# Optimization experiments

Measured on AMD Instinct MI355X. Metric: run time of the kernel, lower is better.

## Reference

```python
import jax, jax.numpy as jnp
import numpy as np

N_EMBD = 2048
N_HEAD = 16
N_KV_HEAD = 4
HEAD_DIM = N_EMBD // N_HEAD  # 128
N_REP = N_HEAD // N_KV_HEAD  # 4
ROPE_BASE = 1000000.0
B, T = 2, 2048


def _rotate_half(x):
    x1, x2 = jnp.split(x, 2, axis=-1)
    return jnp.concatenate([-x2, x1], axis=-1)


def _rope(q, k, t):
    # q: [b,t,h,d], k: [b,t,kvh,d]; full rotary (partial_rotary_factor=1.0)
    pos = jnp.arange(t, dtype=jnp.float32)
    inv_freq = 1.0 / (ROPE_BASE ** (jnp.arange(0, HEAD_DIM, 2, dtype=jnp.float32) / HEAD_DIM))
    ang = pos[:, None] * inv_freq[None, :]                      # [t, d/2]
    cos = jnp.concatenate([jnp.cos(ang), jnp.cos(ang)], -1)     # [t, d]
    sin = jnp.concatenate([jnp.sin(ang), jnp.sin(ang)], -1)
    cos = cos[None, :, None, :]
    sin = sin[None, :, None, :]
    q = q * cos + _rotate_half(q) * sin
    k = k * cos + _rotate_half(k) * sin
    return q, k


def setup_inputs() -> dict:
    key = jax.random.key(0)
    ks = jax.random.split(key, 9)
    std = 0.02
    proj_std = 0.02 / np.sqrt(2 * 24)
    return {
        "x": jax.random.normal(ks[0], (B, T, N_EMBD), dtype=jnp.float32),
        "Wq": jax.random.normal(ks[1], (N_EMBD, N_HEAD * HEAD_DIM), dtype=jnp.float32) * std,
        "bq": jnp.zeros((N_HEAD * HEAD_DIM,), dtype=jnp.float32),
        "Wk": jax.random.normal(ks[2], (N_EMBD, N_KV_HEAD * HEAD_DIM), dtype=jnp.float32) * std,
        "bk": jnp.zeros((N_KV_HEAD * HEAD_DIM,), dtype=jnp.float32),
        "Wv": jax.random.normal(ks[3], (N_EMBD, N_KV_HEAD * HEAD_DIM), dtype=jnp.float32) * std,
        "bv": jnp.zeros((N_KV_HEAD * HEAD_DIM,), dtype=jnp.float32),
        "Wo": jax.random.normal(ks[4], (N_EMBD, N_EMBD), dtype=jnp.float32) * proj_std,
        "bo": jnp.zeros((N_EMBD,), dtype=jnp.float32),
    }


def reference(x, Wq, bq, Wk, bk, Wv, bv, Wo, bo):
    b, t, _ = x.shape
    q = (x @ Wq + bq).reshape(b, t, N_HEAD, HEAD_DIM)
    k = (x @ Wk + bk).reshape(b, t, N_KV_HEAD, HEAD_DIM)
    v = (x @ Wv + bv).reshape(b, t, N_KV_HEAD, HEAD_DIM)
    q, k = _rope(q, k, t)
    # repeat_kv: expand kv heads by n_rep
    k = jnp.broadcast_to(k[:, :, :, None, :], (b, t, N_KV_HEAD, N_REP, HEAD_DIM)).reshape(b, t, N_HEAD, HEAD_DIM)
    v = jnp.broadcast_to(v[:, :, :, None, :], (b, t, N_KV_HEAD, N_REP, HEAD_DIM)).reshape(b, t, N_HEAD, HEAD_DIM)
    qh = q.transpose(0, 2, 1, 3)  # [b,h,t,d]
    kh = k.transpose(0, 2, 1, 3)
    vh = v.transpose(0, 2, 1, 3)
    causal = jnp.tril(jnp.ones((t, t), dtype=bool))[None, None]  # [1,1,t,t]
    bias = jnp.where(causal, 0.0, -1e9).astype(jnp.float32)
    scores = jnp.einsum('bhtd,bhTd->bhtT', qh, kh) / jnp.sqrt(jnp.float32(HEAD_DIM))
    attn_w = jax.nn.softmax(scores + bias, axis=-1)
    attn_out = jnp.einsum('bhtT,bhTd->bhtd', attn_w, vh)
    attn = attn_out.transpose(0, 2, 1, 3).reshape(b, t, N_EMBD)
    return attn @ Wo + bo
```

## Files before the change

### kernel.cpp

```cpp
#include <hip/hip_runtime.h>

typedef _Float16 f16x8 __attribute__((ext_vector_type(8)));
typedef _Float16 f16x4 __attribute__((ext_vector_type(4)));
typedef float    f32x4 __attribute__((ext_vector_type(4)));
typedef float    f32x16 __attribute__((ext_vector_type(16)));
typedef unsigned int u32;
typedef unsigned int u32x2 __attribute__((ext_vector_type(2)));
typedef unsigned int u32x4 __attribute__((ext_vector_type(4)));

__device__ __forceinline__ void gload16(const void* g, void* l) {
  __builtin_amdgcn_global_load_lds((const __attribute__((address_space(1))) void*)g,
                                   (__attribute__((address_space(3))) void*)l, 16, 0, 0);
}

__global__ __launch_bounds__(256) void cast_f32_f16(const float* __restrict__ src,
                                                    _Float16* __restrict__ dst, int n4) {
  int i = blockIdx.x * 256 + threadIdx.x;
  if (i < n4) {
    f32x4 v = *(const f32x4*)(src + (size_t)i * 4);
    f16x4 o;
    o[0] = (_Float16)v[0]; o[1] = (_Float16)v[1];
    o[2] = (_Float16)v[2]; o[3] = (_Float16)v[3];
    *(f16x4*)(dst + (size_t)i * 4) = o;
  }
}

__global__ __launch_bounds__(256) void wqkvtrans_kernel(const float* __restrict__ Wq,
                                                        const float* __restrict__ Wk,
                                                        const float* __restrict__ Wv,
                                                        _Float16* __restrict__ dst) {
  const int n0 = blockIdx.x * 64, k0 = blockIdx.y * 64;
  const float* src; int N, nb;
  if (n0 < 2048)      { src = Wq; N = 2048; nb = n0; }
  else if (n0 < 2560) { src = Wk; N = 512;  nb = n0 - 2048; }
  else                { src = Wv; N = 512;  nb = n0 - 2560; }
  __shared__ float tile[64][65];
#pragma unroll
  for (int i = 0; i < 16; ++i) {
    int id = i * 256 + threadIdx.x;
    int kk = id >> 6, nn = id & 63;
    tile[kk][nn] = src[(size_t)(k0 + kk) * N + nb + nn];
  }
  __syncthreads();
#pragma unroll
  for (int i = 0; i < 16; ++i) {
    int id = i * 256 + threadIdx.x;
    int nn = id >> 6, kk = id & 63;
    dst[(size_t)(n0 + nn) * 2048 + k0 + kk] = (_Float16)tile[kk][nn];
  }
}

__global__ __launch_bounds__(256) void wtrans_kernel(const float* __restrict__ src,
                                                     _Float16* __restrict__ dst,
                                                     int N, int K, int rowOff, int ldDst) {
  const int n0 = blockIdx.x * 64, k0 = blockIdx.y * 64;
  __shared__ float tile[64][65];
#pragma unroll
  for (int i = 0; i < 16; ++i) {
    int id = i * 256 + threadIdx.x;
    int kk = id >> 6, nn = id & 63;
    tile[kk][nn] = src[(size_t)(k0 + kk) * N + n0 + nn];
  }
  __syncthreads();
#pragma unroll
  for (int i = 0; i < 16; ++i) {
    int id = i * 256 + threadIdx.x;
    int nn = id >> 6, kk = id & 63;
    dst[(size_t)(rowOff + n0 + nn) * ldDst + k0 + kk] = (_Float16)tile[kk][nn];
  }
}

__global__ __launch_bounds__(256) void biaspack_kernel(const float* __restrict__ bq,
                                                       const float* __restrict__ bk,
                                                       const float* __restrict__ bv,
                                                       float* __restrict__ out) {
  int i = blockIdx.x * 256 + threadIdx.x;
  if (i < 3072) out[i] = (i < 2048) ? bq[i] : (i < 2560 ? bk[i - 2048] : bv[i - 2560]);
}

__global__ void zeroctr_kernel(int* c) { *c = 0; }

template <bool F16OUT>
__global__ __launch_bounds__(256) void gemm_nt(const _Float16* __restrict__ A,
                                               const _Float16* __restrict__ B,
                                               const float* __restrict__ bias,
                                               void* __restrict__ Cv,
                                               int M, int N, int K) {
  __shared__ __align__(16) _Float16 As[128][64];
  __shared__ __align__(16) _Float16 Bs[128][64];
  const int tid = threadIdx.x;
  const int lane = tid & 63, wave = tid >> 6;
  const int wr = wave >> 1, wc = wave & 1;
  const int r = lane & 15, g = lane >> 4;
  const int rb = blockIdx.y * 128, cb = blockIdx.x * 128;

  const int swz = ((tid & 7) ^ ((tid >> 3) & 7)) * 8;
  const _Float16* aSrc = A + (size_t)(rb + (tid >> 3)) * K + swz;
  const _Float16* bSrc = B + (size_t)(cb + (tid >> 3)) * K + swz;

  f32x4 acc[4][4] = {};

  for (int kt = 0; kt < K; kt += 64) {
    __syncthreads();
#pragma unroll
    for (int p = 0; p < 4; ++p) {
      gload16(aSrc + (size_t)(p * 32) * K + kt, (_Float16*)As + (p * 256 + wave * 64) * 8);
      gload16(bSrc + (size_t)(p * 32) * K + kt, (_Float16*)Bs + (p * 256 + wave * 64) * 8);
    }
    __syncthreads();
#pragma unroll
    for (int kk = 0; kk < 2; ++kk) {
      f16x8 af[4], bf[4];
#pragma unroll
      for (int m = 0; m < 4; ++m) {
        int row = wr * 64 + m * 16 + r;
        af[m] = *(const f16x8*)(&As[row][((kk * 4 + g) ^ (row & 7)) * 8]);
      }
#pragma unroll
      for (int n = 0; n < 4; ++n) {
        int row = wc * 64 + n * 16 + r;
        bf[n] = *(const f16x8*)(&Bs[row][((kk * 4 + g) ^ (row & 7)) * 8]);
      }
#pragma unroll
      for (int m = 0; m < 4; ++m)
#pragma unroll
        for (int n = 0; n < 4; ++n)
          acc[m][n] = __builtin_amdgcn_mfma_f32_16x16x32_f16(af[m], bf[n], acc[m][n], 0, 0, 0);
    }
  }

  float bvals[4];
#pragma unroll
  for (int n = 0; n < 4; ++n) bvals[n] = bias[cb + wc * 64 + n * 16 + r];
#pragma unroll
  for (int m = 0; m < 4; ++m) {
#pragma unroll
    for (int n = 0; n < 4; ++n) {
#pragma unroll
      for (int j = 0; j < 4; ++j) {
        int row = rb + wr * 64 + m * 16 + g * 4 + j;
        int col = cb + wc * 64 + n * 16 + r;
        float v = acc[m][n][j] + bvals[n];
        if (F16OUT)
          ((_Float16*)Cv)[(size_t)row * N + col] = (_Float16)v;
        else
          ((float*)Cv)[(size_t)row * N + col] = v;
      }
    }
  }
}

__global__ __launch_bounds__(256) void rope_kernel(_Float16* __restrict__ QKV) {
  const int tok = blockIdx.x;
  const int t = tok & 2047;
  __shared__ float cs[64], sn[64];
  if (threadIdx.x < 64) {
    int j = threadIdx.x;
    float freq = exp2f((float)(-2 * j) * (19.931568569324174f / 128.0f));
    float ang = (float)t * freq;
    cs[j] = cosf(ang);
    sn[j] = sinf(ang);
  }
  __syncthreads();
  _Float16* base = QKV + (size_t)tok * 3072;
  int idx = threadIdx.x;
  if (idx < 160) {
    int head = idx >> 3, j0 = (idx & 7) * 8;
    int cb = (head < 16) ? head * 128 : 2048 + (head - 16) * 128;
    _Float16* p = base + cb;
    f16x8 a = *(const f16x8*)(p + j0);
    f16x8 b2 = *(const f16x8*)(p + 64 + j0);
    f16x8 oa, ob;
#pragma unroll
    for (int e = 0; e < 8; ++e) {
      float c = cs[j0 + e], s = sn[j0 + e];
      float x1 = (float)a[e], x2 = (float)b2[e];
      oa[e] = (_Float16)(x1 * c - x2 * s);
      ob[e] = (_Float16)(x2 * c + x1 * s);
    }
    *(f16x8*)(p + j0) = oa;
    *(f16x8*)(p + 64 + j0) = ob;
  }
}

__global__ __launch_bounds__(256) void vtrans_kernel(const _Float16* __restrict__ QKV,
                                                     _Float16* __restrict__ Vt) {
  const int bk = blockIdx.z;
  const int t0 = blockIdx.x * 64, d0 = blockIdx.y * 64;
  const int b = bk >> 2, kvh = bk & 3;
  __shared__ _Float16 tile[64][65];
  const _Float16* src = QKV + (size_t)b * 2048 * 3072 + 2560 + kvh * 128;
#pragma unroll
  for (int i = 0; i < 16; ++i) {
    int id = i * 256 + threadIdx.x;
    int tt = id >> 6, dd = id & 63;
    tile[tt][dd] = src[(size_t)(t0 + tt) * 3072 + d0 + dd];
  }
  __syncthreads();
  _Float16* dst = Vt + (size_t)bk * 128 * 2048;
#pragma unroll
  for (int i = 0; i < 16; ++i) {
    int id = i * 256 + threadIdx.x;
    int dd = id >> 6, tt = id & 63;
    dst[(size_t)(d0 + dd) * 2048 + t0 + tt] = tile[tt][dd];
  }
}

__global__ __launch_bounds__(256, 2) void attn_kernel(const _Float16* __restrict__ QKV,
                                                      const _Float16* __restrict__ Vt,
                                                      _Float16* __restrict__ O,
                                                      int* __restrict__ ctr) {
  const int tid = threadIdx.x;
  const int wave = tid >> 6, lane = tid & 63;
  const int l31 = lane & 31, hi = lane >> 5;

  __shared__ __align__(16) _Float16 Klds[2][64][128];
  __shared__ __align__(16) _Float16 Vlds[2][128][64];
  __shared__ int wslot;

  const int kRowOff = tid >> 4, kChunk = ((tid & 15) ^ ((tid >> 4) & 7)) * 8;
  const int vRowOff = tid >> 3, vChunk = ((tid & 7) ^ ((tid >> 3) & 7)) * 8;

  for (;;) {
    __syncthreads();
    if (tid == 0) wslot = atomicAdd(ctr, 1);
    __syncthreads();
    const int w = wslot;
    if (w >= 512) break;
    const int qt = 15 - (w >> 5);
    const int rem = w & 31;
    const int b = rem >> 4, h = rem & 15;
    const int kvh = h >> 2;
    const int q0w = qt * 128 + wave * 32;
    const _Float16* Qb  = QKV + (size_t)b * 2048 * 3072 + h * 128;
    const _Float16* Kb  = QKV + (size_t)b * 2048 * 3072 + 2048 + kvh * 128;
    const _Float16* Vtg = Vt + (size_t)(b * 4 + kvh) * 128 * 2048;
    const _Float16* kSrc = Kb + (size_t)kRowOff * 3072 + kChunk;
    const _Float16* vSrc = Vtg + (size_t)vRowOff * 2048 + vChunk;

    f16x8 qf[8];
    {
      const float qsc = 0.08838834764831845f * 1.4426950408889634f;
      const _Float16* qrow = Qb + (size_t)(q0w + l31) * 3072 + hi * 8;
#pragma unroll
      for (int ds = 0; ds < 8; ++ds) {
        f16x8 v = *(const f16x8*)(qrow + ds * 16);
#pragma unroll
        for (int e = 0; e < 8; ++e) v[e] = (_Float16)((float)v[e] * qsc);
        qf[ds] = v;
      }
    }
    asm volatile("s_waitcnt vmcnt(0)" ::: "memory");

    const int kend = qt * 128 + 128;
    const int qlim = q0w + 32;

    auto stage = [&](int bufi, int kb) {
      _Float16* kd = &Klds[bufi][0][0];
      _Float16* vd = &Vlds[bufi][0][0];
      gload16(kSrc + (size_t)(kb)      * 3072, kd + tid * 8);
      gload16(kSrc + (size_t)(kb + 16) * 3072, kd + (256 + tid) * 8);
      gload16(kSrc + (size_t)(kb + 32) * 3072, kd + (512 + tid) * 8);
      gload16(kSrc + (size_t)(kb + 48) * 3072, kd + (768 + tid) * 8);
      gload16(vSrc + kb,                        vd + tid * 8);
      gload16(vSrc + (size_t)32 * 2048 + kb,    vd + (256 + tid) * 8);
      gload16(vSrc + (size_t)64 * 2048 + kb,    vd + (512 + tid) * 8);
      gload16(vSrc + (size_t)96 * 2048 + kb,    vd + (768 + tid) * 8);
    };

    stage(0, 0);

    f32x16 oacc[4] = {};
    float mrun = -1e30f, lrun = 0.f;
    int cur = 0;

    for (int kb = 0; kb < kend; kb += 64) {
      if (kb + 64 < kend) {
        stage(cur ^ 1, kb + 64);
        asm volatile("s_waitcnt vmcnt(8)" ::: "memory");
      } else {
        asm volatile("s_waitcnt vmcnt(0)" ::: "memory");
      }
      __builtin_amdgcn_s_barrier();
      __builtin_amdgcn_sched_barrier(0);
      if (kb < qlim) {
        f32x16 sT[2] = {};
        __builtin_amdgcn_s_setprio(1);
#pragma unroll
        for (int ds = 0; ds < 8; ++ds) {
#pragma unroll
          for (int ks = 0; ks < 2; ++ks) {
            f16x8 kf = *(const f16x8*)(&Klds[cur][ks * 32 + l31][(((ds * 2 + hi) ^ (l31 & 7)) * 8)]);
            sT[ks] = __builtin_amdgcn_mfma_f32_32x32x16_f16(kf, qf[ds], sT[ks], 0, 0, 0);
          }
        }
        __builtin_amdgcn_s_setprio(0);
        if (kb + 63 > q0w) {
#pragma unroll
          for (int ks = 0; ks < 2; ++ks)
#pragma unroll
            for (int r = 0; r < 16; ++r) {
              int kg = kb + ks * 32 + (r & 3) + 8 * (r >> 2) + 4 * hi;
              if (kg > q0w + l31) sT[ks][r] = -1e30f;
            }
        }
        f32x16 mm;
#pragma unroll
        for (int r = 0; r < 16; ++r) mm[r] = fmaxf(sT[0][r], sT[1][r]);
#pragma unroll
        for (int off = 8; off >= 1; off >>= 1)
#pragma unroll
          for (int r = 0; r < 8; ++r)
            if (r < off) mm[r] = fmaxf(mm[r], mm[r + off]);
        float mt = fmaxf(mm[0], __shfl_xor(mm[0], 32));
        if (__any(mt > mrun)) {
          float mnew = fmaxf(mrun, mt);
          float alpha = exp2f(mrun - mnew);
          lrun *= alpha;
#pragma unroll
          for (int r = 0; r < 16; ++r) {
            float al = __shfl(alpha, (r & 3) + 8 * (r >> 2) + 4 * hi);
#pragma unroll
            for (int dsub = 0; dsub < 4; ++dsub) oacc[dsub][r] *= al;
          }
          mrun = mnew;
        }
        f32x16 ss;
#pragma unroll
        for (int r = 0; r < 16; ++r) {
          sT[0][r] = exp2f(sT[0][r] - mrun);
          sT[1][r] = exp2f(sT[1][r] - mrun);
          ss[r] = sT[0][r] + sT[1][r];
        }
#pragma unroll
        for (int off = 8; off >= 1; off >>= 1)
#pragma unroll
          for (int r = 0; r < 8; ++r)
            if (r < off) ss[r] += ss[r + off];
        lrun += ss[0] + __shfl_xor(ss[0], 32);
        f16x4 q4[8];
#pragma unroll
        for (int m = 0; m < 8; ++m)
#pragma unroll
          for (int t = 0; t < 4; ++t)
            q4[m][t] = (_Float16)sT[m >> 2][(m & 3) * 4 + t];
        f16x8 pa[4];
#pragma unroll
        for (int s = 0; s < 4; ++s) {
          u32x2 wA = __builtin_bit_cast(u32x2, q4[2 * s]);
          u32x2 wB = __builtin_bit_cast(u32x2, q4[2 * s + 1]);
          u32 s0 = hi ? wA.x : wB.x;
          u32 s1 = hi ? wA.y : wB.y;
          u32 r0 = (u32)__shfl_xor((int)s0, 32);
          u32 r1 = (u32)__shfl_xor((int)s1, 32);
          u32 o0 = hi ? wB.x : wA.x;
          u32 o1 = hi ? wB.y : wA.y;
          u32x4 res;
          res.x = hi ? r0 : o0;
          res.y = hi ? r1 : o1;
          res.z = hi ? o0 : r0;
          res.w = hi ? o1 : r1;
          pa[s] = __builtin_bit_cast(f16x8, res);
        }
        __builtin_amdgcn_s_setprio(1);
#pragma unroll
        for (int s = 0; s < 4; ++s) {
#pragma unroll
          for (int dsub = 0; dsub < 4; ++dsub) {
            f16x8 vf = *(const f16x8*)(&Vlds[cur][dsub * 32 + l31][(((s * 2 + hi) ^ (l31 & 7)) * 8)]);
            oacc[dsub] = __builtin_amdgcn_mfma_f32_32x32x16_f16(pa[s], vf, oacc[dsub], 0, 0, 0);
          }
        }
        __builtin_amdgcn_s_setprio(0);
      }
      __builtin_amdgcn_sched_barrier(0);
      __builtin_amdgcn_s_barrier();
      __builtin_amdgcn_sched_barrier(0);
      cur ^= 1;
    }

    float linv = 1.0f / lrun;
#pragma unroll
    for (int r = 0; r < 16; ++r) {
      int qrow = (r & 3) + 8 * (r >> 2) + 4 * hi;
      float li = __shfl(linv, qrow);
      _Float16* orow = O + (size_t)(b * 2048 + q0w + qrow) * 2048 + h * 128 + l31;
#pragma unroll
      for (int dsub = 0; dsub < 4; ++dsub)
        orow[dsub * 32] = (_Float16)(oacc[dsub][r] * li);
    }
  }
}

extern "C" void kernel_launch(void* const* d_in, const int* in_sizes, int n_in,
                              void* d_out, int out_size, void* d_ws, size_t ws_size,
                              hipStream_t stream) {
  const float* x  = (const float*)d_in[0];
  const float* Wq = (const float*)d_in[1];
  const float* bq = (const float*)d_in[2];
  const float* Wk = (const float*)d_in[3];
  const float* bk = (const float*)d_in[4];
  const float* Wv = (const float*)d_in[5];
  const float* bv = (const float*)d_in[6];
  const float* Wo = (const float*)d_in[7];
  const float* bo = (const float*)d_in[8];
  float* out = (float*)d_out;

  char* ws = (char*)d_ws;
  constexpr size_t QKV_OFF  = 0;
  constexpr size_t VT_OFF   = 25165824;
  constexpr size_t ATTN_OFF = VT_OFF + 4194304;
  constexpr size_t WT_OFF   = ATTN_OFF + 16777216;
  constexpr size_t BIAS_OFF = WT_OFF + 12582912;
  constexpr size_t CTR_OFF  = BIAS_OFF + 12288;
  _Float16* QKV  = (_Float16*)(ws + QKV_OFF);
  _Float16* Vt   = (_Float16*)(ws + VT_OFF);
  _Float16* attn = (_Float16*)(ws + ATTN_OFF);
  _Float16* WT   = (_Float16*)(ws + WT_OFF);
  float*    bqkv = (float*)(ws + BIAS_OFF);
  int*      ctr  = (int*)(ws + CTR_OFF);
  _Float16* xb = (_Float16*)d_out;

  cast_f32_f16<<<8192, 256, 0, stream>>>(x, xb, (2 * 2048 * 2048) / 4);
  wqkvtrans_kernel<<<dim3(48, 32), 256, 0, stream>>>(Wq, Wk, Wv, WT);
  biaspack_kernel<<<12, 256, 0, stream>>>(bq, bk, bv, bqkv);
  zeroctr_kernel<<<1, 1, 0, stream>>>(ctr);
  gemm_nt<true><<<dim3(3072 / 128, 4096 / 128), 256, 0, stream>>>(xb, WT, bqkv, QKV, 4096, 3072, 2048);
  wtrans_kernel<<<dim3(32, 32), 256, 0, stream>>>(Wo, WT, 2048, 2048, 0, 2048);
  rope_kernel<<<4096, 256, 0, stream>>>(QKV);
  vtrans_kernel<<<dim3(32, 2, 8), 256, 0, stream>>>(QKV, Vt);
  attn_kernel<<<512, 256, 0, stream>>>(QKV, Vt, attn, ctr);
  gemm_nt<false><<<dim3(2048 / 128, 4096 / 128), 256, 0, stream>>>(attn, WT, bo, out, 4096, 2048, 2048);
}
```

Baseline: 234.5 us.

## Drop attention LDS double-buffering and raise occupancy to four blocks per CU

Replaces the double-buffered K/V LDS staging with a single buffer loaded synchronously at each key block, and raises launch bounds from 2 to 4 blocks per CU. The aim is to hide memory latency through more concurrent blocks instead of software prefetch, since halving LDS use allows more resident workgroups. The trade-off is that each block now stalls on its global-to-LDS loads every iteration. Tighter register limits could also cause spills of the accumulators and Q fragments. The waitcnt after the direct-to-LDS loads was removed, relying on __syncthreads to cover vmcnt, which may be a correctness risk.

After: 301.7 us. +28.6%, slower.

```diff
diff --git a/kernel.cpp b/kernel.cpp
--- a/kernel.cpp
+++ b/kernel.cpp
@@ -206,7 +206,7 @@
   }
 }
 
-__global__ __launch_bounds__(256, 2) void attn_kernel(const _Float16* __restrict__ QKV,
+__global__ __launch_bounds__(256, 4) void attn_kernel(const _Float16* __restrict__ QKV,
                                                       const _Float16* __restrict__ Vt,
                                                       _Float16* __restrict__ O,
                                                       int* __restrict__ ctr) {
@@ -214,8 +214,8 @@
   const int wave = tid >> 6, lane = tid & 63;
   const int l31 = lane & 31, hi = lane >> 5;
 
-  __shared__ __align__(16) _Float16 Klds[2][64][128];
-  __shared__ __align__(16) _Float16 Vlds[2][128][64];
+  __shared__ __align__(16) _Float16 Klds[64][128];
+  __shared__ __align__(16) _Float16 Vlds[128][64];
   __shared__ int wslot;
 
   const int kRowOff = tid >> 4, kChunk = ((tid & 15) ^ ((tid >> 4) & 7)) * 8;
@@ -250,39 +250,23 @@
         qf[ds] = v;
       }
     }
-    asm volatile("s_waitcnt vmcnt(0)" ::: "memory");
 
     const int kend = qt * 128 + 128;
     const int qlim = q0w + 32;
 
-    auto stage = [&](int bufi, int kb) {
-      _Float16* kd = &Klds[bufi][0][0];
-      _Float16* vd = &Vlds[bufi][0][0];
-      gload16(kSrc + (size_t)(kb)      * 3072, kd + tid * 8);
-      gload16(kSrc + (size_t)(kb + 16) * 3072, kd + (256 + tid) * 8);
-      gload16(kSrc + (size_t)(kb + 32) * 3072, kd + (512 + tid) * 8);
-      gload16(kSrc + (size_t)(kb + 48) * 3072, kd + (768 + tid) * 8);
-      gload16(vSrc + kb,                        vd + tid * 8);
-      gload16(vSrc + (size_t)32 * 2048 + kb,    vd + (256 + tid) * 8);
-      gload16(vSrc + (size_t)64 * 2048 + kb,    vd + (512 + tid) * 8);
-      gload16(vSrc + (size_t)96 * 2048 + kb,    vd + (768 + tid) * 8);
-    };
-
-    stage(0, 0);
-
     f32x16 oacc[4] = {};
     float mrun = -1e30f, lrun = 0.f;
-    int cur = 0;
 
     for (int kb = 0; kb < kend; kb += 64) {
-      if (kb + 64 < kend) {
-        stage(cur ^ 1, kb + 64);
-        asm volatile("s_waitcnt vmcnt(8)" ::: "memory");
-      } else {
-        asm volatile("s_waitcnt vmcnt(0)" ::: "memory");
-      }
-      __builtin_amdgcn_s_barrier();
-      __builtin_amdgcn_sched_barrier(0);
+      gload16(kSrc + (size_t)(kb)      * 3072, (_Float16*)Klds + tid * 8);
+      gload16(kSrc + (size_t)(kb + 16) * 3072, (_Float16*)Klds + (256 + tid) * 8);
+      gload16(kSrc + (size_t)(kb + 32) * 3072, (_Float16*)Klds + (512 + tid) * 8);
+      gload16(kSrc + (size_t)(kb + 48) * 3072, (_Float16*)Klds + (768 + tid) * 8);
+      gload16(vSrc + kb,                        (_Float16*)Vlds + tid * 8);
+      gload16(vSrc + (size_t)32 * 2048 + kb,    (_Float16*)Vlds + (256 + tid) * 8);
+      gload16(vSrc + (size_t)64 * 2048 + kb,    (_Float16*)Vlds + (512 + tid) * 8);
+      gload16(vSrc + (size_t)96 * 2048 + kb,    (_Float16*)Vlds + (768 + tid) * 8);
+      __syncthreads();
       if (kb < qlim) {
         f32x16 sT[2] = {};
         __builtin_amdgcn_s_setprio(1);
@@ -290,7 +274,7 @@
         for (int ds = 0; ds < 8; ++ds) {
 #pragma unroll
           for (int ks = 0; ks < 2; ++ks) {
-            f16x8 kf = *(const f16x8*)(&Klds[cur][ks * 32 + l31][(((ds * 2 + hi) ^ (l31 & 7)) * 8)]);
+            f16x8 kf = *(const f16x8*)(&Klds[ks * 32 + l31][(((ds * 2 + hi) ^ (l31 & 7)) * 8)]);
             sT[ks] = __builtin_amdgcn_mfma_f32_32x32x16_f16(kf, qf[ds], sT[ks], 0, 0, 0);
           }
         }
@@ -367,16 +351,13 @@
         for (int s = 0; s < 4; ++s) {
 #pragma unroll
           for (int dsub = 0; dsub < 4; ++dsub) {
-            f16x8 vf = *(const f16x8*)(&Vlds[cur][dsub * 32 + l31][(((s * 2 + hi) ^ (l31 & 7)) * 8)]);
+            f16x8 vf = *(const f16x8*)(&Vlds[dsub * 32 + l31][(((s * 2 + hi) ^ (l31 & 7)) * 8)]);
             oacc[dsub] = __builtin_amdgcn_mfma_f32_32x32x16_f16(pa[s], vf, oacc[dsub], 0, 0, 0);
           }
         }
         __builtin_amdgcn_s_setprio(0);
       }
-      __builtin_amdgcn_sched_barrier(0);
-      __builtin_amdgcn_s_barrier();
-      __builtin_amdgcn_sched_barrier(0);
-      cur ^= 1;
+      __syncthreads();
     }
 
     float linv = 1.0f / lrun;
```
